# Optimization experiments

Hardware: AMD Instinct MI355X
Metric: run time of the kernel (lower is better)

Reference implementation:

```python
import jax, jax.numpy as jnp
import numpy as np

B, T, V, D, H, O = 64, 256, 50000, 512, 1024, 64


def setup_inputs() -> dict:
    key = jax.random.key(0)
    ks = jax.random.split(key, 8)
    s = 1.0 / np.sqrt(H)  # PyTorch GRU/Linear init range
    x = jax.random.randint(ks[0], (B, T), 0, V)
    emb = jax.random.normal(ks[1], (V, D), dtype=jnp.float32) * 0.02
    W_ih = jax.random.uniform(ks[2], (3 * H, D), jnp.float32, -s, s)
    W_hh = jax.random.uniform(ks[3], (3 * H, H), jnp.float32, -s, s)
    b_ih = jax.random.uniform(ks[4], (3 * H,), jnp.float32, -s, s)
    b_hh = jax.random.uniform(ks[5], (3 * H,), jnp.float32, -s, s)
    W_fc = jax.random.uniform(ks[6], (O, H), jnp.float32, -s, s)
    b_fc = jax.random.uniform(ks[7], (O,), jnp.float32, -s, s)
    return {"x": x, "emb": emb, "W_ih": W_ih, "W_hh": W_hh,
            "b_ih": b_ih, "b_hh": b_hh, "W_fc": W_fc, "b_fc": b_fc}


def _gru_seq(gates_x, W_hh, b_hh, h0):
    # gates_x: [T, B, 3H] precomputed input contributions (r|z|n order, as PyTorch)
    def step(h, gx):
        gh = h @ W_hh.T + b_hh                       # [B, 3H]
        xr, xz, xn = jnp.split(gx, 3, axis=-1)
        hr, hz, hn = jnpp_split(gh) if False else jnp.split(gh, 3, axis=-1)
        r = jax.nn.sigmoid(xr + hr)
        z = jax.nn.sigmoid(xz + hz)
        n = jnp.tanh(xn + r * hn)
        h_new = (1.0 - z) * n + z * h
        return h_new, h_new

    _, hs = jax.lax.scan(step, h0, gates_x)          # hs: [T, B, H]
    return hs


def reference(x, emb, W_ih, W_hh, b_ih, b_hh, W_fc, b_fc):
    xe = emb[x]                                      # [B, T, D]
    # Precompute all input-to-gate projections in one GEMM: [B, T, 3H]
    gates_x = jnp.einsum('btd,gd->btg', xe, W_ih) + b_ih
    h0 = jnp.zeros((x.shape[0], W_hh.shape[1]), dtype=xe.dtype)
    hs = _gru_seq(jnp.swapaxes(gates_x, 0, 1), W_hh, b_hh, h0)  # [T, B, H]
    out = jnp.swapaxes(hs, 0, 1)                     # [B, T, H]
    logits = jnp.einsum('bth,oh->bto', out, W_fc) + b_fc
    proba = jax.nn.sigmoid(logits)
    predicted_labels = (proba > 0.5).astype(jnp.float32)
    return proba, predicted_labels
```

## Files before the change

kernel.cpp:

```cpp
#include <hip/hip_runtime.h>
#include <math.h>

#define B_   64
#define T_   256
#define D_   512
#define H_   1024
#define G3_  3072
#define O_   64
#define NTOK (B_*T_)
#define TC_  64
#define NCH_ 4

__global__ __launch_bounds__(256) void init_ws(double* __restrict__ hs,
                                               int* __restrict__ flags)
{
  int idx = blockIdx.x*256 + threadIdx.x;
  hs[idx] = 0.0;
  if (idx < 4096) flags[idx] = 0;
}

__global__ __launch_bounds__(256) void stage_a(
    const int* __restrict__ x, const float* __restrict__ emb,
    const float* __restrict__ W_ih, const float* __restrict__ b_ih,
    double* __restrict__ gx, int t_base)
{
  __shared__ float As[64][33];
  __shared__ float Bs[64][33];
  const int tid = threadIdx.x;
  const int b = blockIdx.x & 63, nBlk = blockIdx.x >> 6;
  const int g0 = nBlk*64;

  const int r = tid >> 2, c8 = tid & 3;
  const float* ap = emb  + (size_t)x[b*T_ + t_base + r]*D_ + c8*8;
  const float* bp = W_ih + (size_t)(g0 + r)*D_ + c8*8;
  const int tx = tid & 15, ty = tid >> 4;

  double acc[4][4];
  #pragma unroll
  for (int i = 0; i < 4; ++i)
    #pragma unroll
    for (int j = 0; j < 4; ++j) acc[i][j] = 0.0;

  float4 a0 = *(const float4*)(ap), a1 = *(const float4*)(ap + 4);
  float4 b0 = *(const float4*)(bp), b1 = *(const float4*)(bp + 4);

  for (int kb = 0; kb < 16; ++kb){
    __syncthreads();
    As[r][c8*8+0]=a0.x; As[r][c8*8+1]=a0.y; As[r][c8*8+2]=a0.z; As[r][c8*8+3]=a0.w;
    As[r][c8*8+4]=a1.x; As[r][c8*8+5]=a1.y; As[r][c8*8+6]=a1.z; As[r][c8*8+7]=a1.w;
    Bs[r][c8*8+0]=b0.x; Bs[r][c8*8+1]=b0.y; Bs[r][c8*8+2]=b0.z; Bs[r][c8*8+3]=b0.w;
    Bs[r][c8*8+4]=b1.x; Bs[r][c8*8+5]=b1.y; Bs[r][c8*8+6]=b1.z; Bs[r][c8*8+7]=b1.w;
    __syncthreads();
    if (kb < 15){
      a0 = *(const float4*)(ap + (kb+1)*32);  a1 = *(const float4*)(ap + (kb+1)*32 + 4);
      b0 = *(const float4*)(bp + (kb+1)*32);  b1 = *(const float4*)(bp + (kb+1)*32 + 4);
    }
    #pragma unroll
    for (int k = 0; k < 32; ++k){
      double av[4], bv[4];
      #pragma unroll
      for (int i = 0; i < 4; ++i) av[i] = (double)As[ty*4+i][k];
      #pragma unroll
      for (int j = 0; j < 4; ++j) bv[j] = (double)Bs[tx*4+j][k];
      #pragma unroll
      for (int i = 0; i < 4; ++i)
        #pragma unroll
        for (int j = 0; j < 4; ++j) acc[i][j] = fma(av[i], bv[j], acc[i][j]);
    }
  }

  double bi[4];
  #pragma unroll
  for (int j = 0; j < 4; ++j) bi[j] = (double)b_ih[g0 + tx*4 + j];
  #pragma unroll
  for (int i = 0; i < 4; ++i){
    int tl = ty*4 + i;
    size_t rowoff = ((size_t)tl*B_ + b)*G3_ + g0 + tx*4;
    #pragma unroll
    for (int j = 0; j < 4; ++j)
      gx[rowoff + j] = acc[i][j] + bi[j];
  }
}

__global__ __launch_bounds__(256, 1) void gru_rec(
    const float* __restrict__ W_hh, const float* __restrict__ b_hh,
    const double* __restrict__ gx, double* __restrict__ hs,
    int* __restrict__ flags, int t_base)
{
  __shared__ float Wf[2*12*516];
  __shared__ int abort_flag;
  const int tid = threadIdx.x, wg = blockIdx.x;
  const int i0 = wg*4;
  if (tid == 0) abort_flag = 0;

  for (int it = tid; it < 12*1024; it += 256){
    int rr = it >> 10, k = it & 1023;
    int p = rr >> 2, j = rr & 3;
    int hf = k >> 9, kl = k & 511;
    Wf[(hf*12 + rr)*516 + kl] = W_hh[(size_t)(p*H_ + i0 + j)*H_ + k];
  }

  const int bq = tid >> 3, j = (tid >> 1) & 3, half = tid & 1;
  const int b_out = bq*2 + half;
  const int jj = i0 + j;
  const double bh0 = (double)b_hh[jj];
  const double bh1 = (double)b_hh[H_   + jj];
  const double bh2 = (double)b_hh[2*H_ + jj];
  const float4* w0p = (const float4*)&Wf[(half*12 + 0*4 + j)*516];
  const float4* w1p = (const float4*)&Wf[(half*12 + 1*4 + j)*516];
  const float4* w2p = (const float4*)&Wf[(half*12 + 2*4 + j)*516];
  __syncthreads();

  double hprev = hs[(size_t)b_out*H_ + jj];

  for (int tt = 0; tt < TC_; ++tt){
    const int t = t_base + tt;

    const double* gp = gx + ((size_t)tt*B_ + b_out)*G3_ + jj;
    double gxr = gp[0];
    double gxz = gp[H_];
    double gxn = gp[2*H_];

    {
      int* fp = flags + tid*16;
      int gcnt = 0;
      while (__hip_atomic_load(fp, __ATOMIC_RELAXED, __HIP_MEMORY_SCOPE_AGENT) < t){
        __builtin_amdgcn_s_sleep(2);
        if (++gcnt > (1<<18)) { abort_flag = 1; break; }
      }
    }
    __syncthreads();
    if (abort_flag) break;

    const double2* h0 = (const double2*)(hs + ((size_t)tt*B_ + bq*2    )*H_ + half*512);
    const double2* h1 = (const double2*)(hs + ((size_t)tt*B_ + bq*2 + 1)*H_ + half*512);

    double pr00=0.0, pr10=0.0, pr20=0.0, pr01=0.0, pr11=0.0, pr21=0.0;
    #pragma unroll 16
    for (int kk = 0; kk < 128; ++kk){
      double2 a00 = h0[2*kk], a01 = h0[2*kk+1];
      double2 a10 = h1[2*kk], a11 = h1[2*kk+1];
      float4 w0 = w0p[kk];
      float4 w1 = w1p[kk];
      float4 w2 = w2p[kk];
      double w0x=(double)w0.x, w0y=(double)w0.y, w0z=(double)w0.z, w0w=(double)w0.w;
      double w1x=(double)w1.x, w1y=(double)w1.y, w1z=(double)w1.z, w1w=(double)w1.w;
      double w2x=(double)w2.x, w2y=(double)w2.y, w2z=(double)w2.z, w2w=(double)w2.w;
      pr00 = fma(a00.x, w0x, pr00); pr00 = fma(a00.y, w0y, pr00);
      pr00 = fma(a01.x, w0z, pr00); pr00 = fma(a01.y, w0w, pr00);
      pr10 = fma(a00.x, w1x, pr10); pr10 = fma(a00.y, w1y, pr10);
      pr10 = fma(a01.x, w1z, pr10); pr10 = fma(a01.y, w1w, pr10);
      pr20 = fma(a00.x, w2x, pr20); pr20 = fma(a00.y, w2y, pr20);
      pr20 = fma(a01.x, w2z, pr20); pr20 = fma(a01.y, w2w, pr20);
      pr01 = fma(a10.x, w0x, pr01); pr01 = fma(a10.y, w0y, pr01);
      pr01 = fma(a11.x, w0z, pr01); pr01 = fma(a11.y, w0w, pr01);
      pr11 = fma(a10.x, w1x, pr11); pr11 = fma(a10.y, w1y, pr11);
      pr11 = fma(a11.x, w1z, pr11); pr11 = fma(a11.y, w1w, pr11);
      pr21 = fma(a10.x, w2x, pr21); pr21 = fma(a10.y, w2y, pr21);
      pr21 = fma(a11.x, w2z, pr21); pr21 = fma(a11.y, w2w, pr21);
    }
    double s00 = pr00 + __shfl_xor(pr00, 1);
    double s01 = pr01 + __shfl_xor(pr01, 1);
    double s10 = pr10 + __shfl_xor(pr10, 1);
    double s11 = pr11 + __shfl_xor(pr11, 1);
    double s20 = pr20 + __shfl_xor(pr20, 1);
    double s21 = pr21 + __shfl_xor(pr21, 1);
    double ar = half ? s01 : s00;
    double az = half ? s11 : s10;
    double an = half ? s21 : s20;

    double rr_ = 1.0/(1.0 + exp(-(gxr + ar + bh0)));
    double zz  = 1.0/(1.0 + exp(-(gxz + az + bh1)));
    double nn  = tanh(gxn + rr_*(an + bh2));
    double hnew = (1.0 - zz)*nn + zz*hprev;
    hprev = hnew;

    __hip_atomic_store(&hs[((size_t)(tt+1)*B_ + b_out)*H_ + jj], hnew,
                       __ATOMIC_RELAXED, __HIP_MEMORY_SCOPE_AGENT);
    if (tt == TC_-1)
      __hip_atomic_store(&hs[(size_t)b_out*H_ + jj], hnew,
                         __ATOMIC_RELAXED, __HIP_MEMORY_SCOPE_AGENT);

    asm volatile("s_waitcnt vmcnt(0)" ::: "memory");
    __syncthreads();
    if (tid == 0)
      __hip_atomic_store(flags + wg*16, t+1, __ATOMIC_RELAXED, __HIP_MEMORY_SCOPE_AGENT);
  }
}

__global__ __launch_bounds__(256) void fc_out(
    const double* __restrict__ hs, const float* __restrict__ W_fc,
    const float* __restrict__ b_fc, float* __restrict__ out, int t_base)
{
  __shared__ double Ah[64][34];
  __shared__ double Bw[64][34];
  const int tid = threadIdx.x;
  const int b = blockIdx.x;
  const int r = tid >> 2, c8 = tid & 3;
  const double* ap = hs   + ((size_t)(r+1)*B_ + b)*H_ + c8*8;
  const float*  bp = W_fc + (size_t)r*H_ + c8*8;
  const int tx = tid & 15, ty = tid >> 4;

  double acc[4][4];
  #pragma unroll
  for (int i = 0; i < 4; ++i)
    #pragma unroll
    for (int j = 0; j < 4; ++j) acc[i][j] = 0.0;

  double ar0[8]; float br0[8];
  #pragma unroll
  for (int e = 0; e < 8; ++e){ ar0[e] = ap[e]; br0[e] = bp[e]; }

  for (int kb = 0; kb < 32; ++kb){
    __syncthreads();
    #pragma unroll
    for (int e = 0; e < 8; ++e){
      Ah[r][c8*8+e] = ar0[e];
      Bw[r][c8*8+e] = (double)br0[e];
    }
    __syncthreads();
    if (kb < 31){
      #pragma unroll
      for (int e = 0; e < 8; ++e){
        ar0[e] = ap[(kb+1)*32 + e];
        br0[e] = bp[(kb+1)*32 + e];
      }
    }
    #pragma unroll
    for (int k = 0; k < 32; ++k){
      double av[4], bv[4];
      #pragma unroll
      for (int i = 0; i < 4; ++i) av[i] = Ah[ty*4+i][k];
      #pragma unroll
      for (int j = 0; j < 4; ++j) bv[j] = Bw[tx*4+j][k];
      #pragma unroll
      for (int i = 0; i < 4; ++i)
        #pragma unroll
        for (int j = 0; j < 4; ++j) acc[i][j] = fma(av[i], bv[j], acc[i][j]);
    }
  }

  double bi[4];
  #pragma unroll
  for (int j = 0; j < 4; ++j) bi[j] = (double)b_fc[tx*4 + j];
  #pragma unroll
  for (int i = 0; i < 4; ++i){
    int tl = ty*4 + i;
    size_t tok = (size_t)b*T_ + t_base + tl;
    float4 pr, lb;
    float* prp = (float*)&pr; float* lbp = (float*)&lb;
    #pragma unroll
    for (int j = 0; j < 4; ++j){
      double logit = acc[i][j] + bi[j];
      prp[j] = (float)(1.0/(1.0 + exp(-logit)));
      float lf = (float)logit;
      float ef = (float)exp(-(double)lf);
      float pf = 1.0f / (1.0f + ef);
      lbp[j] = (pf > 0.5f) ? 1.0f : 0.0f;
    }
    *(float4*)&out[tok*O_ + tx*4] = pr;
    *(float4*)&out[(size_t)NTOK*O_ + tok*O_ + tx*4] = lb;
  }
}

extern "C" void kernel_launch(void* const* d_in, const int* in_sizes, int n_in,
                              void* d_out, int out_size, void* d_ws, size_t ws_size,
                              hipStream_t stream) {
  const int*   x    = (const int*)  d_in[0];
  const float* emb  = (const float*)d_in[1];
  const float* W_ih = (const float*)d_in[2];
  const float* W_hh = (const float*)d_in[3];
  const float* b_ih = (const float*)d_in[4];
  const float* b_hh = (const float*)d_in[5];
  const float* W_fc = (const float*)d_in[6];
  const float* b_fc = (const float*)d_in[7];
  float* out = (float*)d_out;
  char* ws = (char*)d_ws;

  double* gx    = (double*)(ws);
  double* hs    = (double*)(ws + 100663296);
  int*    flags = (int*)   (ws + 134742016);

  hipLaunchKernelGGL(init_ws, dim3(256), dim3(256), 0, stream, hs, flags);
  for (int c = 0; c < NCH_; ++c){
    int t_base = c*TC_;
    hipLaunchKernelGGL(stage_a, dim3(3072), dim3(256), 0, stream,
                       x, emb, W_ih, b_ih, gx, t_base);
    hipLaunchKernelGGL(gru_rec, dim3(256), dim3(256), 0, stream,
                       W_hh, b_hh, gx, hs, flags, t_base);
    hipLaunchKernelGGL(fc_out, dim3(64), dim3(256), 0, stream,
                       hs, W_fc, b_fc, out, t_base);
  }
}
```

Measured before the change: 10.64 ms.

## Split GRU recurrence across 512 workgroups with quarter-K reduction per thread

The persistent recurrent kernel now uses 512 workgroups, each owning 2 hidden units instead of 4. The K dimension is split four ways across lanes, with an extra shuffle reduction, so each thread does half as many FMAs per step. Every workgroup now polls twice as many flags at each timestep barrier. The goal is to use all CUs and shorten per-step latency, at the cost of heavier grid-wide synchronization and a co-residency requirement of 2 blocks per CU.

```diff
diff --git a/kernel.cpp b/kernel.cpp
--- a/kernel.cpp
+++ b/kernel.cpp
@@ -16,7 +16,7 @@
 {
   int idx = blockIdx.x*256 + threadIdx.x;
   hs[idx] = 0.0;
-  if (idx < 4096) flags[idx] = 0;
+  if (idx < 8192) flags[idx] = 0;
 }
 
 __global__ __launch_bounds__(256) void stage_a(
@@ -82,33 +82,33 @@
   }
 }
 
-__global__ __launch_bounds__(256, 1) void gru_rec(
+__global__ __launch_bounds__(256, 2) void gru_rec(
     const float* __restrict__ W_hh, const float* __restrict__ b_hh,
     const double* __restrict__ gx, double* __restrict__ hs,
     int* __restrict__ flags, int t_base)
 {
-  __shared__ float Wf[2*12*516];
+  __shared__ float Wf[6*4*260];
   __shared__ int abort_flag;
   const int tid = threadIdx.x, wg = blockIdx.x;
-  const int i0 = wg*4;
+  const int i0 = wg*2;
   if (tid == 0) abort_flag = 0;
 
-  for (int it = tid; it < 12*1024; it += 256){
+  for (int it = tid; it < 6*1024; it += 256){
     int rr = it >> 10, k = it & 1023;
-    int p = rr >> 2, j = rr & 3;
-    int hf = k >> 9, kl = k & 511;
-    Wf[(hf*12 + rr)*516 + kl] = W_hh[(size_t)(p*H_ + i0 + j)*H_ + k];
-  }
-
-  const int bq = tid >> 3, j = (tid >> 1) & 3, half = tid & 1;
-  const int b_out = bq*2 + half;
+    int p = rr >> 1, j = rr & 1;
+    Wf[(rr*4 + (k >> 8))*260 + (k & 255)] = W_hh[(size_t)(p*H_ + i0 + j)*H_ + k];
+  }
+
+  const int bq = tid >> 3, j = (tid >> 2) & 1, quarter = tid & 3;
+  const int b_out = bq*2 + (quarter & 1);
+  const bool owner = (quarter < 2);
   const int jj = i0 + j;
   const double bh0 = (double)b_hh[jj];
   const double bh1 = (double)b_hh[H_   + jj];
   const double bh2 = (double)b_hh[2*H_ + jj];
-  const float4* w0p = (const float4*)&Wf[(half*12 + 0*4 + j)*516];
-  const float4* w1p = (const float4*)&Wf[(half*12 + 1*4 + j)*516];
-  const float4* w2p = (const float4*)&Wf[(half*12 + 2*4 + j)*516];
+  const float4* w0p = (const float4*)&Wf[((0*2 + j)*4 + quarter)*260];
+  const float4* w1p = (const float4*)&Wf[((1*2 + j)*4 + quarter)*260];
+  const float4* w2p = (const float4*)&Wf[((2*2 + j)*4 + quarter)*260];
   __syncthreads();
 
   double hprev = hs[(size_t)b_out*H_ + jj];
@@ -122,9 +122,11 @@
     double gxn = gp[2*H_];
 
     {
-      int* fp = flags + tid*16;
+      int* fp1 = flags + tid*16;
+      int* fp2 = flags + (tid + 256)*16;
       int gcnt = 0;
-      while (__hip_atomic_load(fp, __ATOMIC_RELAXED, __HIP_MEMORY_SCOPE_AGENT) < t){
+      while (__hip_atomic_load(fp1, __ATOMIC_RELAXED, __HIP_MEMORY_SCOPE_AGENT) < t ||
+             __hip_atomic_load(fp2, __ATOMIC_RELAXED, __HIP_MEMORY_SCOPE_AGENT) < t){
         __builtin_amdgcn_s_sleep(2);
         if (++gcnt > (1<<18)) { abort_flag = 1; break; }
       }
@@ -132,12 +134,12 @@
     __syncthreads();
     if (abort_flag) break;
 
-    const double2* h0 = (const double2*)(hs + ((size_t)tt*B_ + bq*2    )*H_ + half*512);
-    const double2* h1 = (const double2*)(hs + ((size_t)tt*B_ + bq*2 + 1)*H_ + half*512);
+    const double2* h0 = (const double2*)(hs + ((size_t)tt*B_ + bq*2    )*H_ + quarter*256);
+    const double2* h1 = (const double2*)(hs + ((size_t)tt*B_ + bq*2 + 1)*H_ + quarter*256);
 
     double pr00=0.0, pr10=0.0, pr20=0.0, pr01=0.0, pr11=0.0, pr21=0.0;
-    #pragma unroll 16
-    for (int kk = 0; kk < 128; ++kk){
+    #pragma unroll 8
+    for (int kk = 0; kk < 64; ++kk){
       double2 a00 = h0[2*kk], a01 = h0[2*kk+1];
       double2 a10 = h1[2*kk], a11 = h1[2*kk+1];
       float4 w0 = w0p[kk];
@@ -159,15 +161,15 @@
       pr21 = fma(a10.x, w2x, pr21); pr21 = fma(a10.y, w2y, pr21);
       pr21 = fma(a11.x, w2z, pr21); pr21 = fma(a11.y, w2w, pr21);
     }
-    double s00 = pr00 + __shfl_xor(pr00, 1);
-    double s01 = pr01 + __shfl_xor(pr01, 1);
-    double s10 = pr10 + __shfl_xor(pr10, 1);
-    double s11 = pr11 + __shfl_xor(pr11, 1);
-    double s20 = pr20 + __shfl_xor(pr20, 1);
-    double s21 = pr21 + __shfl_xor(pr21, 1);
-    double ar = half ? s01 : s00;
-    double az = half ? s11 : s10;
-    double an = half ? s21 : s20;
+    double s00 = pr00 + __shfl_xor(pr00, 1); s00 += __shfl_xor(s00, 2);
+    double s01 = pr01 + __shfl_xor(pr01, 1); s01 += __shfl_xor(s01, 2);
+    double s10 = pr10 + __shfl_xor(pr10, 1); s10 += __shfl_xor(s10, 2);
+    double s11 = pr11 + __shfl_xor(pr11, 1); s11 += __shfl_xor(s11, 2);
+    double s20 = pr20 + __shfl_xor(pr20, 1); s20 += __shfl_xor(s20, 2);
+    double s21 = pr21 + __shfl_xor(pr21, 1); s21 += __shfl_xor(s21, 2);
+    double ar = (quarter & 1) ? s01 : s00;
+    double az = (quarter & 1) ? s11 : s10;
+    double an = (quarter & 1) ? s21 : s20;
 
     double rr_ = 1.0/(1.0 + exp(-(gxr + ar + bh0)));
     double zz  = 1.0/(1.0 + exp(-(gxz + az + bh1)));
@@ -175,11 +177,13 @@
     double hnew = (1.0 - zz)*nn + zz*hprev;
     hprev = hnew;
 
-    __hip_atomic_store(&hs[((size_t)(tt+1)*B_ + b_out)*H_ + jj], hnew,
-                       __ATOMIC_RELAXED, __HIP_MEMORY_SCOPE_AGENT);
-    if (tt == TC_-1)
-      __hip_atomic_store(&hs[(size_t)b_out*H_ + jj], hnew,
+    if (owner){
+      __hip_atomic_store(&hs[((size_t)(tt+1)*B_ + b_out)*H_ + jj], hnew,
                          __ATOMIC_RELAXED, __HIP_MEMORY_SCOPE_AGENT);
+      if (tt == TC_-1)
+        __hip_atomic_store(&hs[(size_t)b_out*H_ + jj], hnew,
+                           __ATOMIC_RELAXED, __HIP_MEMORY_SCOPE_AGENT);
+    }
 
     asm volatile("s_waitcnt vmcnt(0)" ::: "memory");
     __syncthreads();
@@ -286,7 +290,7 @@
     int t_base = c*TC_;
     hipLaunchKernelGGL(stage_a, dim3(3072), dim3(256), 0, stream,
                        x, emb, W_ih, b_ih, gx, t_base);
-    hipLaunchKernelGGL(gru_rec, dim3(256), dim3(256), 0, stream,
+    hipLaunchKernelGGL(gru_rec, dim3(512), dim3(256), 0, stream,
                        W_hh, b_hh, gx, hs, flags, t_base);
     hipLaunchKernelGGL(fc_out, dim3(64), dim3(256), 0, stream,
                        hs, W_fc, b_fc, out, t_base);
```

After: 17.54 ms. +64.7%, slower.
